# Kernel optimization log

Measured on AMD Instinct MI355X. Metric: run time of the kernel, lower is better.

## Reference

```python
import jax, jax.numpy as jnp
import numpy as np

VOCAB, D_WORD, D_TOPIC, D_NOUN_HIDDEN = 50000, 300, 128, 312
B, L = 8192, 32
N_MONTH = D_NOUN_HIDDEN - D_WORD  # 12


def setup_inputs() -> dict:
    key = jax.random.key(0)
    ks = jax.random.split(key, 8)
    return {
        "topic_emb": jax.random.normal(ks[0], (D_TOPIC,), dtype=jnp.float32),
        "noun_ids": jax.random.randint(ks[1], (B, L), 0, VOCAB),
        "lengths": jax.random.randint(ks[2], (B,), 0, 33),
        "months": jax.random.randint(ks[3], (B,), 0, N_MONTH),
        "month_info_encode": 1,
        "we": jax.random.normal(ks[4], (VOCAB, D_WORD), dtype=jnp.float32),
        "k_w": jax.random.normal(ks[5], (D_TOPIC, D_NOUN_HIDDEN), dtype=jnp.float32) * (1.0 / np.sqrt(D_NOUN_HIDDEN)),
        "k_b": jnp.zeros((D_TOPIC,), dtype=jnp.float32),
        "q_w": jax.random.normal(ks[6], (D_TOPIC, D_TOPIC), dtype=jnp.float32) * (1.0 / np.sqrt(D_TOPIC)),
        "q_b": jnp.zeros((D_TOPIC,), dtype=jnp.float32),
    }


def reference(topic_emb, noun_ids, lengths, months, month_info_encode, we, k_w, k_b, q_w, q_b):
    # Ragged per-sample loop collapsed into one padded+masked batch pass.
    Bn, Ln = noun_ids.shape
    d_topic = q_w.shape[0]
    emb = we[noun_ids]  # [B, L, d_word] embedding lookup
    # one-hot month features, broadcast over tokens: [B, L, N_MONTH]
    month_oh = jax.nn.one_hot(months, N_MONTH, dtype=emb.dtype) * jnp.asarray(month_info_encode, emb.dtype)
    month_part = jnp.broadcast_to(month_oh[:, None, :], (Bn, Ln, N_MONTH))
    value = jnp.concatenate([emb, month_part], axis=-1)  # [B, L, Dh]
    key = value @ k_w.T + k_b                            # [B, L, d_topic]
    query = topic_emb @ q_w.T + q_b                      # [d_topic]
    scale = 1.0 / jnp.sqrt(jnp.asarray(d_topic, value.dtype))
    scores = jnp.einsum('bld,d->bl', key, query) * scale  # [B, L]
    valid = jnp.arange(Ln)[None, :] < lengths[:, None]    # ragged mask
    attn = jax.nn.softmax(jnp.where(valid, scores, -1e9), axis=-1)
    out = jnp.einsum('bl,bld->bd', attn, value)           # [B, Dh]
    # samples with empty spans stay zero (original leaves outputs[i] = 0)
    return jnp.where((lengths > 0)[:, None], out, jnp.zeros_like(out))
```

## Files before the change

### kernel.cpp

```cpp
#include <hip/hip_runtime.h>
#include <math.h>

#define VOCAB 50000
#define D_WORD 300
#define D_TOPIC 128
#define DH 312
#define NB 8192
#define LMAX 32
#define N_MONTH 12

__device__ __forceinline__ float wave_sum_uniform(float x) {
    int v = __float_as_int(x);
    int t;
#define DPP_STEP(ctrl)                                                   \
    t = __builtin_amdgcn_update_dpp(0, v, (ctrl), 0xf, 0xf, true);       \
    v = __float_as_int(__int_as_float(v) + __int_as_float(t));
    DPP_STEP(0x111)
    DPP_STEP(0x112)
    DPP_STEP(0x114)
    DPP_STEP(0x118)
    DPP_STEP(0x142)
    DPP_STEP(0x143)
#undef DPP_STEP
    return __int_as_float(__builtin_amdgcn_readlane(v, 63));
}

__global__ __launch_bounds__(320) void compute_w_kernel(
    const float* __restrict__ topic_emb,
    const float* __restrict__ q_w, const float* __restrict__ q_b,
    const float* __restrict__ k_w,
    float* __restrict__ w_out)
{
    __shared__ float query_s[D_TOPIC];
    __shared__ float topic_s[D_TOPIC];
    int t = threadIdx.x;
    if (t < D_TOPIC) topic_s[t] = topic_emb[t];
    __syncthreads();
    if (t < D_TOPIC) {
        const float4* qr = (const float4*)(q_w + t * D_TOPIC);
        float q0 = q_b[t], q1 = 0.f, q2 = 0.f, q3 = 0.f;
        #pragma unroll 8
        for (int k4 = 0; k4 < D_TOPIC / 4; ++k4) {
            float4 v = qr[k4];
            q0 = fmaf(v.x, topic_s[4 * k4 + 0], q0);
            q1 = fmaf(v.y, topic_s[4 * k4 + 1], q1);
            q2 = fmaf(v.z, topic_s[4 * k4 + 2], q2);
            q3 = fmaf(v.w, topic_s[4 * k4 + 3], q3);
        }
        query_s[t] = (q0 + q1) + (q2 + q3);
    }
    __syncthreads();
    if (t < DH) {
        float a0 = 0.f, a1 = 0.f, a2 = 0.f, a3 = 0.f;
        #pragma unroll 8
        for (int d = 0; d < D_TOPIC; d += 4) {
            a0 = fmaf(k_w[(d + 0) * DH + t], query_s[d + 0], a0);
            a1 = fmaf(k_w[(d + 1) * DH + t], query_s[d + 1], a1);
            a2 = fmaf(k_w[(d + 2) * DH + t], query_s[d + 2], a2);
            a3 = fmaf(k_w[(d + 3) * DH + t], query_s[d + 3], a3);
        }
        w_out[t] = ((a0 + a1) + (a2 + a3)) * 0.08838834764831845f;
    }
}

__global__ __launch_bounds__(256) void attn_fused_kernel(
    const int* __restrict__ noun_ids, const int* __restrict__ lengths,
    const int* __restrict__ months, const int* __restrict__ encode_p,
    const float* __restrict__ we, const float* __restrict__ w,
    float* __restrict__ out)
{
    int wave = threadIdx.x >> 6, lane = threadIdx.x & 63;
    int b = blockIdx.x * 4 + wave;
    float4* ob = (float4*)(out + (size_t)b * DH);
    int len = lengths[b];

    if (len <= 0) {
        float4 z = {0.f, 0.f, 0.f, 0.f};
        ob[lane] = z;
        if (lane < 14) ob[64 + lane] = z;
        return;
    }
    if (len > LMAX) len = LMAX;

    const float4* w4 = (const float4*)w;
    float4 ww = w4[lane];
    float4 wb = (lane < 11) ? w4[64 + lane] : (float4){0.f, 0.f, 0.f, 0.f};

    int id = (lane < LMAX) ? noun_ids[b * LMAX + lane] : 0;

    float m = -1e30f, denom = 0.f;
    float4 acc0 = {0.f, 0.f, 0.f, 0.f};
    float4 acc1 = {0.f, 0.f, 0.f, 0.f};
    const float4 z4 = {0.f, 0.f, 0.f, 0.f};

    bool cdual = (len > 1);
    {
        int rid0 = __shfl(id, 0);
        int rid1 = __shfl(id, cdual ? 1 : 0);
        const float4* r0 = (const float4*)(we + (size_t)rid0 * D_WORD);
        const float4* r1 = (const float4*)(we + (size_t)rid1 * D_WORD);
        float4 cA0 = r0[lane];
        float4 cB0 = r1[lane];
        float4 cA1 = (lane < 11) ? r0[64 + lane] : z4;
        float4 cB1 = (lane < 11) ? r1[64 + lane] : z4;

        for (int l = 0; l < len; l += 2) {
            int nl = (l + 2 < len) ? l + 2 : l;
            bool ndual = (nl + 1 < len);
            int nrid0 = __shfl(id, nl);
            int nrid1 = __shfl(id, ndual ? nl + 1 : nl);
            const float4* nr0 = (const float4*)(we + (size_t)nrid0 * D_WORD);
            const float4* nr1 = (const float4*)(we + (size_t)nrid1 * D_WORD);
            float4 nA0 = nr0[lane];
            float4 nB0 = nr1[lane];
            float4 nA1 = (lane < 11) ? nr0[64 + lane] : z4;
            float4 nB1 = (lane < 11) ? nr1[64 + lane] : z4;

            float p0 = fmaf(cA0.x, ww.x, fmaf(cA0.y, ww.y,
                       fmaf(cA0.z, ww.z, fmaf(cA0.w, ww.w,
                       fmaf(cA1.x, wb.x, fmaf(cA1.y, wb.y,
                       fmaf(cA1.z, wb.z, cA1.w * wb.w)))))));
            float p1 = fmaf(cB0.x, ww.x, fmaf(cB0.y, ww.y,
                       fmaf(cB0.z, ww.z, fmaf(cB0.w, ww.w,
                       fmaf(cB1.x, wb.x, fmaf(cB1.y, wb.y,
                       fmaf(cB1.z, wb.z, cB1.w * wb.w)))))));
            p0 = wave_sum_uniform(p0);
            p1 = wave_sum_uniform(p1);
            if (!cdual) p1 = -1e30f;

            float mn = fmaxf(fmaxf(m, p0), p1);
            float c  = __expf(m  - mn);
            float e0 = __expf(p0 - mn);
            float e1 = __expf(p1 - mn);
            m = mn;
            denom = fmaf(denom, c, e0 + e1);
            acc0.x = fmaf(acc0.x, c, fmaf(e0, cA0.x, e1 * cB0.x));
            acc0.y = fmaf(acc0.y, c, fmaf(e0, cA0.y, e1 * cB0.y));
            acc0.z = fmaf(acc0.z, c, fmaf(e0, cA0.z, e1 * cB0.z));
            acc0.w = fmaf(acc0.w, c, fmaf(e0, cA0.w, e1 * cB0.w));
            acc1.x = fmaf(acc1.x, c, fmaf(e0, cA1.x, e1 * cB1.x));
            acc1.y = fmaf(acc1.y, c, fmaf(e0, cA1.y, e1 * cB1.y));
            acc1.z = fmaf(acc1.z, c, fmaf(e0, cA1.z, e1 * cB1.z));
            acc1.w = fmaf(acc1.w, c, fmaf(e0, cA1.w, e1 * cB1.w));

            cA0 = nA0; cB0 = nB0; cA1 = nA1; cB1 = nB1; cdual = ndual;
        }
    }

    float rs = 1.f / denom;
    acc0.x *= rs; acc0.y *= rs; acc0.z *= rs; acc0.w *= rs;
    ob[lane] = acc0;
    if (lane < 11) {
        acc1.x *= rs; acc1.y *= rs; acc1.z *= rs; acc1.w *= rs;
        ob[64 + lane] = acc1;
    } else if (lane < 14) {
        int mo = months[b];
        float enc = (float)(*encode_p);
        int base = (lane - 11) * 4;
        float4 oh;
        oh.x = (base + 0 == mo) ? enc : 0.f;
        oh.y = (base + 1 == mo) ? enc : 0.f;
        oh.z = (base + 2 == mo) ? enc : 0.f;
        oh.w = (base + 3 == mo) ? enc : 0.f;
        ob[64 + lane] = oh;
    }
}

extern "C" void kernel_launch(void* const* d_in, const int* in_sizes, int n_in,
                              void* d_out, int out_size, void* d_ws, size_t ws_size,
                              hipStream_t stream) {
    const float* topic_emb = (const float*)d_in[0];
    const int*   noun_ids  = (const int*)d_in[1];
    const int*   lengths   = (const int*)d_in[2];
    const int*   months    = (const int*)d_in[3];
    const int*   encode    = (const int*)d_in[4];
    const float* we        = (const float*)d_in[5];
    const float* k_w       = (const float*)d_in[6];
    const float* q_w       = (const float*)d_in[8];
    const float* q_b       = (const float*)d_in[9];
    float* out = (float*)d_out;

    float* w_vec = (float*)d_ws;

    compute_w_kernel<<<1, 320, 0, stream>>>(topic_emb, q_w, q_b, k_w, w_vec);
    attn_fused_kernel<<<NB / 4, 256, 0, stream>>>(noun_ids, lengths, months,
                                                  encode, we, w_vec, out);
}
```

Baseline: 132.3 us.

## Fold log2e into w, use raw exp2, readlane ids, split w kernel

Multiplies the precomputed scoring vector by log2(e) so the online softmax can call the hardware exp2 intrinsic directly instead of __expf. Token ids are now broadcast with readlane in place of shuffles, and a launch-bounds occupancy hint is added to the attention kernel. The small w-precompute kernel is split across 4 blocks of 128 threads, and each block recomputes the query vector redundantly. The main kernel is bound by gathering embedding rows from memory, so these ALU-side changes are unlikely to matter much.

```diff
diff --git a/kernel.cpp b/kernel.cpp
--- a/kernel.cpp
+++ b/kernel.cpp
@@ -25,7 +25,11 @@
     return __int_as_float(__builtin_amdgcn_readlane(v, 63));
 }
 
-__global__ __launch_bounds__(320) void compute_w_kernel(
+__device__ __forceinline__ float fexp2(float x) {
+    return __builtin_amdgcn_exp2f(x);
+}
+
+__global__ __launch_bounds__(128) void compute_w_kernel(
     const float* __restrict__ topic_emb,
     const float* __restrict__ q_w, const float* __restrict__ q_b,
     const float* __restrict__ k_w,
@@ -34,9 +38,9 @@
     __shared__ float query_s[D_TOPIC];
     __shared__ float topic_s[D_TOPIC];
     int t = threadIdx.x;
-    if (t < D_TOPIC) topic_s[t] = topic_emb[t];
+    topic_s[t] = topic_emb[t];
     __syncthreads();
-    if (t < D_TOPIC) {
+    {
         const float4* qr = (const float4*)(q_w + t * D_TOPIC);
         float q0 = q_b[t], q1 = 0.f, q2 = 0.f, q3 = 0.f;
         #pragma unroll 8
@@ -50,20 +54,22 @@
         query_s[t] = (q0 + q1) + (q2 + q3);
     }
     __syncthreads();
-    if (t < DH) {
+    if (t < 78) {
+        int o = blockIdx.x * 78 + t;
         float a0 = 0.f, a1 = 0.f, a2 = 0.f, a3 = 0.f;
         #pragma unroll 8
         for (int d = 0; d < D_TOPIC; d += 4) {
-            a0 = fmaf(k_w[(d + 0) * DH + t], query_s[d + 0], a0);
-            a1 = fmaf(k_w[(d + 1) * DH + t], query_s[d + 1], a1);
-            a2 = fmaf(k_w[(d + 2) * DH + t], query_s[d + 2], a2);
-            a3 = fmaf(k_w[(d + 3) * DH + t], query_s[d + 3], a3);
+            a0 = fmaf(k_w[(d + 0) * DH + o], query_s[d + 0], a0);
+            a1 = fmaf(k_w[(d + 1) * DH + o], query_s[d + 1], a1);
+            a2 = fmaf(k_w[(d + 2) * DH + o], query_s[d + 2], a2);
+            a3 = fmaf(k_w[(d + 3) * DH + o], query_s[d + 3], a3);
         }
-        w_out[t] = ((a0 + a1) + (a2 + a3)) * 0.08838834764831845f;
+        w_out[o] = ((a0 + a1) + (a2 + a3))
+                 * (0.08838834764831845f * 1.4426950408889634f);
     }
 }
 
-__global__ __launch_bounds__(256) void attn_fused_kernel(
+__global__ __launch_bounds__(256, 4) void attn_fused_kernel(
     const int* __restrict__ noun_ids, const int* __restrict__ lengths,
     const int* __restrict__ months, const int* __restrict__ encode_p,
     const float* __restrict__ we, const float* __restrict__ w,
@@ -95,8 +101,8 @@
 
     bool cdual = (len > 1);
     {
-        int rid0 = __shfl(id, 0);
-        int rid1 = __shfl(id, cdual ? 1 : 0);
+        int rid0 = __builtin_amdgcn_readlane(id, 0);
+        int rid1 = __builtin_amdgcn_readlane(id, cdual ? 1 : 0);
         const float4* r0 = (const float4*)(we + (size_t)rid0 * D_WORD);
         const float4* r1 = (const float4*)(we + (size_t)rid1 * D_WORD);
         float4 cA0 = r0[lane];
@@ -107,8 +113,8 @@
         for (int l = 0; l < len; l += 2) {
             int nl = (l + 2 < len) ? l + 2 : l;
             bool ndual = (nl + 1 < len);
-            int nrid0 = __shfl(id, nl);
-            int nrid1 = __shfl(id, ndual ? nl + 1 : nl);
+            int nrid0 = __builtin_amdgcn_readlane(id, nl);
+            int nrid1 = __builtin_amdgcn_readlane(id, ndual ? nl + 1 : nl);
             const float4* nr0 = (const float4*)(we + (size_t)nrid0 * D_WORD);
             const float4* nr1 = (const float4*)(we + (size_t)nrid1 * D_WORD);
             float4 nA0 = nr0[lane];
@@ -129,9 +135,9 @@
             if (!cdual) p1 = -1e30f;
 
             float mn = fmaxf(fmaxf(m, p0), p1);
-            float c  = __expf(m  - mn);
-            float e0 = __expf(p0 - mn);
-            float e1 = __expf(p1 - mn);
+            float c  = fexp2(m  - mn);
+            float e0 = fexp2(p0 - mn);
+            float e1 = fexp2(p1 - mn);
             m = mn;
             denom = fmaf(denom, c, e0 + e1);
             acc0.x = fmaf(acc0.x, c, fmaf(e0, cA0.x, e1 * cB0.x));
@@ -182,7 +188,7 @@
 
     float* w_vec = (float*)d_ws;
 
-    compute_w_kernel<<<1, 320, 0, stream>>>(topic_emb, q_w, q_b, k_w, w_vec);
+    compute_w_kernel<<<4, 128, 0, stream>>>(topic_emb, q_w, q_b, k_w, w_vec);
     attn_fused_kernel<<<NB / 4, 256, 0, stream>>>(noun_ids, lengths, months,
                                                   encode, we, w_vec, out);
 }
```

Measured after the change: 133.2 us. About the same (+0.7%).
